# Kernel optimization log

Hardware: AMD Instinct MI355X
Metric: run time of the kernel (lower is better)

## Reference

```python
import jax, jax.numpy as jnp
import numpy as np

B, C, H, W = 4, 256, 64, 64
CR = max(C // 8, 1)  # reduced channels
EPS = 1e-12  # F.normalize eps


def setup_inputs() -> dict:
    key = jax.random.key(0)
    ks = jax.random.split(key, 8)
    s = 1.0 / np.sqrt(C)
    return {
        "x": jax.random.normal(ks[0], (B, C, H, W), dtype=jnp.float32),
        "Wq": jax.random.normal(ks[1], (CR, C), dtype=jnp.float32) * s,
        "bq": jax.random.normal(ks[2], (CR,), dtype=jnp.float32) * s,
        "Wk": jax.random.normal(ks[3], (CR, C), dtype=jnp.float32) * s,
        "bk": jax.random.normal(ks[4], (CR,), dtype=jnp.float32) * s,
        "Wv": jax.random.normal(ks[5], (C, C), dtype=jnp.float32) * s,
        "bv": jax.random.normal(ks[6], (C,), dtype=jnp.float32) * s,
        "gamma": jax.random.normal(ks[7], (1,), dtype=jnp.float32),
    }


def reference(x, Wq, bq, Wk, bk, Wv, bv, gamma):
    b, c, h, w = x.shape
    xf = x.reshape(b, c, h * w)  # [B, C, N]
    # 1x1 convs are per-pixel linear maps
    q = jnp.einsum("rc,bcn->brn", Wq, xf) + bq[None, :, None]  # [B, CR, N]
    k = jnp.einsum("rc,bcn->brn", Wk, xf) + bk[None, :, None]  # [B, CR, N]
    v = jnp.einsum("dc,bcn->bdn", Wv, xf) + bv[None, :, None]  # [B, C, N]
    # attention = bmm(key^T, query): [B, N, N]
    attn = jnp.einsum("brn,brm->bnm", k, q)
    attn = jax.nn.relu(attn)
    # L1 normalize along dim=1 (rows), matching F.normalize(p=1, dim=1)
    denom = jnp.maximum(jnp.sum(jnp.abs(attn), axis=1, keepdims=True), EPS)
    attn = attn / denom
    out = jnp.einsum("bcn,bnm->bcm", v, attn).reshape(b, c, h, w)
    return gamma[0] * out + x
```

## Files before the change

kernel.cpp:

```cpp
#include <hip/hip_runtime.h>
#include <hip/hip_bf16.h>

#define NB 4
#define NC 256
#define NN 4096
#define NCR 32

typedef __attribute__((ext_vector_type(8))) short short8_t;
typedef __attribute__((ext_vector_type(4))) float f32x4;
typedef __attribute__((ext_vector_type(2))) int int2_t;
typedef __attribute__((ext_vector_type(4))) int int4_t;
typedef __attribute__((ext_vector_type(4))) float float4_t;

static __device__ __forceinline__ unsigned short f2bf(float f) {
  unsigned u = __builtin_bit_cast(unsigned, f);
  u += 0x7FFFu + ((u >> 16) & 1u);
  return (unsigned short)(u >> 16);
}

static __device__ __forceinline__ unsigned cvt_pk(float lo, float hi) {
  unsigned r;
  asm("v_cvt_pk_bf16_f32 %0, %1, %2" : "=v"(r) : "v"(lo), "v"(hi));
  return r;
}

__global__ __launch_bounds__(64) void pack_w_kernel(
    const float* __restrict__ Wq, const float* __restrict__ Wk,
    const float* __restrict__ Wv, unsigned short* __restrict__ Wbf)
{
  const int row = blockIdx.x;
  const int t = threadIdx.x;
  const float* src = row < 32 ? Wq + (size_t)row * NC
                   : (row < 64 ? Wk + (size_t)(row - 32) * NC
                               : Wv + (size_t)(row - 64) * NC);
  float4_t v = *(const float4_t*)(src + t * 4);
  int2_t p;
  p[0] = cvt_pk(v[0], v[1]);
  p[1] = cvt_pk(v[2], v[3]);
  *(int2_t*)(Wbf + (size_t)row * NC + t * 4) = p;
}

__global__ __launch_bounds__(256) void qkv_kernel(
    const float* __restrict__ x, const unsigned short* __restrict__ Wbf,
    const float* __restrict__ bq, const float* __restrict__ bk,
    const float* __restrict__ bv,
    unsigned short* __restrict__ Qt, unsigned short* __restrict__ Kt,
    unsigned short* __restrict__ Vt)
{
  __shared__ unsigned short xT[2][64 * 32];

  const int bid = blockIdx.x;
  const int b   = bid >> 6;
  const int m0  = (bid & 63) * 64;
  const int tid = threadIdx.x;
  const int w    = tid >> 6;
  const int lane = tid & 63;
  const int lg   = lane >> 4;
  const int lm   = lane & 15;

  const float* xb = x + (size_t)b * NC * NN;
  const float* xld = xb + (size_t)(8 * w) * NN + m0 + lane;
  const int wofs = lane * 32 + ((w ^ (lane & 3)) << 3);
  const unsigned short* wrow = Wbf + (size_t)(w * 80 + lm) * NC;

  const f32x4 zero4 = {0.f, 0.f, 0.f, 0.f};
  f32x4 acc[5][4];
#pragma unroll
  for (int df = 0; df < 5; df++)
#pragma unroll
    for (int mf = 0; mf < 4; mf++) acc[df][mf] = zero4;

  float xg[8], xn[8];
#pragma unroll
  for (int j = 0; j < 8; j++) xg[j] = xld[j * NN];

#define QSTEP(KC, XC, XN, BUF) {                                              \
    if ((KC) < 7) {                                                           \
      _Pragma("unroll") for (int j = 0; j < 8; j++)                           \
        XN[j] = xld[(((KC) + 1) * 32 + j) * NN];                              \
    }                                                                         \
    short8_t wf[5];                                                           \
    _Pragma("unroll") for (int df = 0; df < 5; df++)                          \
      wf[df] = *(const short8_t*)(wrow + df * 16 * NC + (KC) * 32 + lg * 8);  \
    int4_t xw;                                                                \
    xw[0] = cvt_pk(XC[0], XC[1]); xw[1] = cvt_pk(XC[2], XC[3]);               \
    xw[2] = cvt_pk(XC[4], XC[5]); xw[3] = cvt_pk(XC[6], XC[7]);               \
    *(int4_t*)(&xT[BUF][wofs]) = xw;                                          \
    __syncthreads();                                                          \
    short8_t xf[4];                                                           \
    _Pragma("unroll") for (int mf = 0; mf < 4; mf++)                          \
      xf[mf] = *(const short8_t*)(&xT[BUF][(mf * 16 + lm) * 32 +              \
                                          ((lg ^ (lm & 3)) << 3)]);           \
    _Pragma("unroll") for (int df = 0; df < 5; df++)                          \
      _Pragma("unroll") for (int mf = 0; mf < 4; mf++)                        \
        acc[df][mf] = __builtin_amdgcn_mfma_f32_16x16x32_bf16(                \
            xf[mf], wf[df], acc[df][mf], 0, 0, 0);                            \
  }

#pragma unroll
  for (int kc = 0; kc < 8; kc += 2) {
    QSTEP(kc, xg, xn, 0)
    QSTEP(kc + 1, xn, xg, 1)
  }
#undef QSTEP

#pragma unroll
  for (int df = 0; df < 5; df++) {
    const int dbase = w * 80 + df * 16;
    if (dbase < 64) {
      const bool isq = dbase < 32;
      const float bia = isq ? bq[dbase + lm] : bk[dbase - 32 + lm];
      unsigned short* dst = isq ? Qt : Kt;
      const int dcol = (isq ? dbase : dbase - 32) + lm;
#pragma unroll
      for (int mf = 0; mf < 4; mf++)
#pragma unroll
        for (int i = 0; i < 4; i++) {
          const int m = m0 + mf * 16 + lg * 4 + i;
          dst[((size_t)b * NN + m) * NCR + dcol] = f2bf(acc[df][mf][i] + bia);
        }
    } else {
      const int c = dbase - 64 + lm;
      const float bia = bv[c];
#pragma unroll
      for (int mf = 0; mf < 4; mf++) {
        int2_t p;
        p[0] = cvt_pk(acc[df][mf][0] + bia, acc[df][mf][1] + bia);
        p[1] = cvt_pk(acc[df][mf][2] + bia, acc[df][mf][3] + bia);
        *(int2_t*)(Vt + ((size_t)b * NC + c) * NN + m0 + mf * 16 + lg * 4) = p;
      }
    }
  }
}

__global__ __launch_bounds__(256) void attn_kernel(
    const unsigned short* __restrict__ Qt, const unsigned short* __restrict__ Kt,
    const unsigned short* __restrict__ Vt, const float* __restrict__ x,
    const float* __restrict__ gamma, float* __restrict__ out)
{
  __shared__ unsigned short Slds[2][64 * 72];
  __shared__ float dlds[4][64];

  int bid = blockIdx.x;
  bid = (bid & 7) * 32 + (bid >> 3);
  const int b   = bid >> 6;
  const int m0  = (bid & 63) * 64;
  const int tid = threadIdx.x;
  const int w    = tid >> 6;
  const int lane = tid & 63;
  const int lg   = lane >> 4;
  const int lm   = lane & 15;

  const unsigned short* Qb = Qt + (size_t)b * NN * NCR;
  const unsigned short* Kb = Kt + (size_t)b * NN * NCR + (w * 16 + lm) * NCR + lg * 8;
  const unsigned short* Vb = Vt + (size_t)b * NC * NN;
  const unsigned short* pV[4];
#pragma unroll
  for (int cf = 0; cf < 4; cf++)
    pV[cf] = Vb + (size_t)(w * 64 + cf * 16 + lm) * NN + lg * 8;

  short8_t qf[4];
#pragma unroll
  for (int mf = 0; mf < 4; mf++)
    qf[mf] = *(const short8_t*)(Qb + (size_t)(m0 + mf * 16 + lm) * NCR + lg * 8);

  const f32x4 zero4 = {0.f, 0.f, 0.f, 0.f};
  f32x4 acc[4][4];
#pragma unroll
  for (int cf = 0; cf < 4; cf++)
#pragma unroll
    for (int mf = 0; mf < 4; mf++) acc[cf][mf] = zero4;
  float dsum[4] = {0.f, 0.f, 0.f, 0.f};

  short8_t kA, kB, vA[4][2], vB[4][2];
  kA = *(const short8_t*)(Kb);
#pragma unroll
  for (int cf = 0; cf < 4; cf++)
#pragma unroll
    for (int nch = 0; nch < 2; nch++)
      vA[cf][nch] = *(const short8_t*)(pV[cf] + nch * 32);

  const int swofs = w * 16 + lg * 4;

#define AITER(T, VC, VN, KC, KN, BUF) {                                       \
    const int n1 = (((T) + 1) & 63) * 64;                                     \
    KN = *(const short8_t*)(Kb + (size_t)n1 * NCR);                           \
    _Pragma("unroll") for (int cf = 0; cf < 4; cf++)                          \
      _Pragma("unroll") for (int nch = 0; nch < 2; nch++)                     \
        VN[cf][nch] = *(const short8_t*)(pV[cf] + n1 + nch * 32);             \
    _Pragma("unroll") for (int mf = 0; mf < 4; mf++) {                        \
      f32x4 s = __builtin_amdgcn_mfma_f32_16x16x32_bf16(KC, qf[mf], zero4, 0, 0, 0); \
      float s0 = fmaxf(s[0], 0.f), s1 = fmaxf(s[1], 0.f);                     \
      float s2 = fmaxf(s[2], 0.f), s3 = fmaxf(s[3], 0.f);                     \
      dsum[mf] += (s0 + s1) + (s2 + s3);                                      \
      int2_t p; p[0] = cvt_pk(s0, s1); p[1] = cvt_pk(s2, s3);                 \
      *(int2_t*)(&Slds[BUF][(mf * 16 + lm) * 72 + swofs]) = p;                \
    }                                                                         \
    __syncthreads();                                                          \
    _Pragma("unroll") for (int nch = 0; nch < 2; nch++) {                     \
      short8_t sf[4];                                                         \
      _Pragma("unroll") for (int mf = 0; mf < 4; mf++)                        \
        sf[mf] = *(const short8_t*)(&Slds[BUF][(mf * 16 + lm) * 72 + nch * 32 + lg * 8]); \
      _Pragma("unroll") for (int cf = 0; cf < 4; cf++)                        \
        _Pragma("unroll") for (int mf = 0; mf < 4; mf++)                      \
          acc[cf][mf] = __builtin_amdgcn_mfma_f32_16x16x32_bf16(              \
              VC[cf][nch], sf[mf], acc[cf][mf], 0, 0, 0);                     \
    }                                                                         \
  }

#pragma unroll 1
  for (int t = 0; t < 64; t += 2) {
    AITER(t, vA, vB, kA, kB, 0)
    AITER(t + 1, vB, vA, kB, kA, 1)
  }
#undef AITER

#pragma unroll
  for (int mf = 0; mf < 4; mf++) {
    float v = dsum[mf];
    v += __shfl_xor(v, 16);
    v += __shfl_xor(v, 32);
    dsum[mf] = v;
  }
  if (lane < 16) {
#pragma unroll
    for (int mf = 0; mf < 4; mf++) dlds[w][mf * 16 + lane] = dsum[mf];
  }
  __syncthreads();

  const float g0 = gamma[0];
  float rden[4];
#pragma unroll
  for (int mf = 0; mf < 4; mf++) {
    const int mloc = mf * 16 + lm;
    float den = dlds[0][mloc] + dlds[1][mloc] + dlds[2][mloc] + dlds[3][mloc];
    den = den > 1e-12f ? den : 1e-12f;
    rden[mf] = 1.0f / den;
  }

  const float* xb = x + (size_t)b * NC * NN;
  float* ob = out + (size_t)b * NC * NN;
#pragma unroll
  for (int cf = 0; cf < 4; cf++) {
#pragma unroll
    for (int i = 0; i < 4; i++) {
      const int c = w * 64 + cf * 16 + lg * 4 + i;
#pragma unroll
      for (int mf = 0; mf < 4; mf++) {
        const int m = m0 + mf * 16 + lm;
        ob[(size_t)c * NN + m] = g0 * acc[cf][mf][i] * rden[mf] + xb[(size_t)c * NN + m];
      }
    }
  }
}

extern "C" void kernel_launch(void* const* d_in, const int* in_sizes, int n_in,
                              void* d_out, int out_size, void* d_ws, size_t ws_size,
                              hipStream_t stream) {
  const float* x     = (const float*)d_in[0];
  const float* Wq    = (const float*)d_in[1];
  const float* bq    = (const float*)d_in[2];
  const float* Wk    = (const float*)d_in[3];
  const float* bk    = (const float*)d_in[4];
  const float* Wv    = (const float*)d_in[5];
  const float* bv    = (const float*)d_in[6];
  const float* gamma = (const float*)d_in[7];
  float* out = (float*)d_out;

  unsigned short* Wbf = (unsigned short*)d_ws;
  unsigned short* Qt  = Wbf + (size_t)320 * NC;
  unsigned short* Kt  = Qt + (size_t)NB * NN * NCR;
  unsigned short* Vt  = Kt + (size_t)NB * NN * NCR;

  hipLaunchKernelGGL(pack_w_kernel, dim3(320), dim3(64), 0, stream,
                     Wq, Wk, Wv, Wbf);
  hipLaunchKernelGGL(qkv_kernel, dim3(256), dim3(256), 0, stream,
                     x, Wbf, bq, bk, bv, Qt, Kt, Vt);
  hipLaunchKernelGGL(attn_kernel, dim3(256), dim3(256), 0, stream,
                     Qt, Kt, Vt, x, gamma, out);
}
```

Before: 88.24 us.

## Split attention key range across 8 waves and halve QKV tile per block

The attention kernel now runs 512 threads per block. Waves 4-7 process the second half of each 128-key tile, and the two halves' accumulators are reduced through LDS at the end, with s_setprio raised around the MFMA phase. The QKV projection kernel uses 32-pixel tiles over 512 blocks with a wider K chunk and a new swizzle. The aim is more waves in flight to hide the latency of V/K loads on a 256-block grid, at the cost of extra LDS traffic and synchronisation for the cross-wave reduction.

After: 211.7 us. 2.4x slower.

```diff
diff --git a/kernel.cpp b/kernel.cpp
--- a/kernel.cpp
+++ b/kernel.cpp
@@ -5,6 +5,7 @@
 #define NC 256
 #define NN 4096
 #define NCR 32
+#define PITCH 136
 
 typedef __attribute__((ext_vector_type(8))) short short8_t;
 typedef __attribute__((ext_vector_type(4))) float f32x4;
@@ -40,69 +41,72 @@
   *(int2_t*)(Wbf + (size_t)row * NC + t * 4) = p;
 }
 
-__global__ __launch_bounds__(256) void qkv_kernel(
+__global__ __launch_bounds__(256, 2) void qkv_kernel(
     const float* __restrict__ x, const unsigned short* __restrict__ Wbf,
     const float* __restrict__ bq, const float* __restrict__ bk,
     const float* __restrict__ bv,
     unsigned short* __restrict__ Qt, unsigned short* __restrict__ Kt,
     unsigned short* __restrict__ Vt)
 {
-  __shared__ unsigned short xT[2][64 * 32];
+  __shared__ unsigned short xT[2][32 * 64];
 
   const int bid = blockIdx.x;
-  const int b   = bid >> 6;
-  const int m0  = (bid & 63) * 64;
+  const int b   = bid >> 7;
+  const int m0  = (bid & 127) * 32;
   const int tid = threadIdx.x;
   const int w    = tid >> 6;
   const int lane = tid & 63;
   const int lg   = lane >> 4;
   const int lm   = lane & 15;
 
-  const float* xb = x + (size_t)b * NC * NN;
-  const float* xld = xb + (size_t)(8 * w) * NN + m0 + lane;
-  const int wofs = lane * 32 + ((w ^ (lane & 3)) << 3);
+  const int mcol = tid & 31, kg = tid >> 5;
+  const float* xld = x + (size_t)b * NC * NN + (size_t)(kg * 8) * NN + m0 + mcol;
+  const int wofs = mcol * 64 + ((kg ^ (mcol & 7)) << 3);
   const unsigned short* wrow = Wbf + (size_t)(w * 80 + lm) * NC;
 
   const f32x4 zero4 = {0.f, 0.f, 0.f, 0.f};
-  f32x4 acc[5][4];
+  f32x4 acc[5][2];
 #pragma unroll
   for (int df = 0; df < 5; df++)
 #pragma unroll
-    for (int mf = 0; mf < 4; mf++) acc[df][mf] = zero4;
+    for (int mf = 0; mf < 2; mf++) acc[df][mf] = zero4;
 
   float xg[8], xn[8];
 #pragma unroll
-  for (int j = 0; j < 8; j++) xg[j] = xld[j * NN];
-
-#define QSTEP(KC, XC, XN, BUF) {                                              \
-    if ((KC) < 7) {                                                           \
+  for (int j = 0; j < 8; j++) xg[j] = xld[(size_t)j * NN];
+
+#define QCHUNK(C, XC, XN, BUF) {                                              \
+    if ((C) < 3) {                                                            \
       _Pragma("unroll") for (int j = 0; j < 8; j++)                           \
-        XN[j] = xld[(((KC) + 1) * 32 + j) * NN];                              \
+        XN[j] = xld[(size_t)(((C) + 1) * 64 + j) * NN];                       \
     }                                                                         \
-    short8_t wf[5];                                                           \
-    _Pragma("unroll") for (int df = 0; df < 5; df++)                          \
-      wf[df] = *(const short8_t*)(wrow + df * 16 * NC + (KC) * 32 + lg * 8);  \
-    int4_t xw;                                                                \
-    xw[0] = cvt_pk(XC[0], XC[1]); xw[1] = cvt_pk(XC[2], XC[3]);               \
-    xw[2] = cvt_pk(XC[4], XC[5]); xw[3] = cvt_pk(XC[6], XC[7]);               \
-    *(int4_t*)(&xT[BUF][wofs]) = xw;                                          \
+    int4_t xwv;                                                               \
+    xwv[0] = cvt_pk(XC[0], XC[1]); xwv[1] = cvt_pk(XC[2], XC[3]);             \
+    xwv[2] = cvt_pk(XC[4], XC[5]); xwv[3] = cvt_pk(XC[6], XC[7]);             \
+    *(int4_t*)(&xT[BUF][wofs]) = xwv;                                         \
     __syncthreads();                                                          \
-    short8_t xf[4];                                                           \
-    _Pragma("unroll") for (int mf = 0; mf < 4; mf++)                          \
-      xf[mf] = *(const short8_t*)(&xT[BUF][(mf * 16 + lm) * 32 +              \
-                                          ((lg ^ (lm & 3)) << 3)]);           \
-    _Pragma("unroll") for (int df = 0; df < 5; df++)                          \
-      _Pragma("unroll") for (int mf = 0; mf < 4; mf++)                        \
-        acc[df][mf] = __builtin_amdgcn_mfma_f32_16x16x32_bf16(                \
-            xf[mf], wf[df], acc[df][mf], 0, 0, 0);                            \
-  }
-
-#pragma unroll
-  for (int kc = 0; kc < 8; kc += 2) {
-    QSTEP(kc, xg, xn, 0)
-    QSTEP(kc + 1, xn, xg, 1)
-  }
-#undef QSTEP
+    _Pragma("unroll") for (int ks = 0; ks < 2; ks++) {                        \
+      short8_t xf[2];                                                         \
+      _Pragma("unroll") for (int mf = 0; mf < 2; mf++) {                      \
+        const int row = mf * 16 + lm;                                         \
+        const int unit = (ks * 4 + lg) ^ (lm & 7);                            \
+        xf[mf] = *(const short8_t*)(&xT[BUF][row * 64 + unit * 8]);           \
+      }                                                                       \
+      _Pragma("unroll") for (int df = 0; df < 5; df++) {                      \
+        const short8_t wf = *(const short8_t*)(wrow + (size_t)df * 16 * NC +  \
+                                               (C) * 64 + ks * 32 + lg * 8);  \
+        _Pragma("unroll") for (int mf = 0; mf < 2; mf++)                      \
+          acc[df][mf] = __builtin_amdgcn_mfma_f32_16x16x32_bf16(              \
+              xf[mf], wf, acc[df][mf], 0, 0, 0);                              \
+      }                                                                       \
+    }                                                                         \
+  }
+
+  QCHUNK(0, xg, xn, 0)
+  QCHUNK(1, xn, xg, 1)
+  QCHUNK(2, xg, xn, 0)
+  QCHUNK(3, xn, xg, 1)
+#undef QCHUNK
 
 #pragma unroll
   for (int df = 0; df < 5; df++) {
@@ -113,7 +117,7 @@
       unsigned short* dst = isq ? Qt : Kt;
       const int dcol = (isq ? dbase : dbase - 32) + lm;
 #pragma unroll
-      for (int mf = 0; mf < 4; mf++)
+      for (int mf = 0; mf < 2; mf++)
 #pragma unroll
         for (int i = 0; i < 4; i++) {
           const int m = m0 + mf * 16 + lg * 4 + i;
@@ -123,7 +127,7 @@
       const int c = dbase - 64 + lm;
       const float bia = bv[c];
 #pragma unroll
-      for (int mf = 0; mf < 4; mf++) {
+      for (int mf = 0; mf < 2; mf++) {
         int2_t p;
         p[0] = cvt_pk(acc[df][mf][0] + bia, acc[df][mf][1] + bia);
         p[1] = cvt_pk(acc[df][mf][2] + bia, acc[df][mf][3] + bia);
@@ -133,13 +137,14 @@
   }
 }
 
-__global__ __launch_bounds__(256) void attn_kernel(
+__global__ __launch_bounds__(512, 2) void attn_kernel(
     const unsigned short* __restrict__ Qt, const unsigned short* __restrict__ Kt,
     const unsigned short* __restrict__ Vt, const float* __restrict__ x,
     const float* __restrict__ gamma, float* __restrict__ out)
 {
-  __shared__ unsigned short Slds[2][64 * 72];
-  __shared__ float dlds[4][64];
+  __shared__ unsigned short Slds[2][64 * PITCH];
+  __shared__ float mbuf[4][64][17];
+  __shared__ float dlds[8][64];
 
   int bid = blockIdx.x;
   bid = (bid & 7) * 32 + (bid >> 3);
@@ -150,14 +155,17 @@
   const int lane = tid & 63;
   const int lg   = lane >> 4;
   const int lm   = lane & 15;
+  const int cg   = w & 3;
+  const int nh   = w >> 2;
 
   const unsigned short* Qb = Qt + (size_t)b * NN * NCR;
-  const unsigned short* Kb = Kt + (size_t)b * NN * NCR + (w * 16 + lm) * NCR + lg * 8;
+  const unsigned short* Kp = Kt + (size_t)b * NN * NCR +
+                             (size_t)(w * 16 + lm) * NCR + lg * 8;
   const unsigned short* Vb = Vt + (size_t)b * NC * NN;
   const unsigned short* pV[4];
 #pragma unroll
   for (int cf = 0; cf < 4; cf++)
-    pV[cf] = Vb + (size_t)(w * 64 + cf * 16 + lm) * NN + lg * 8;
+    pV[cf] = Vb + (size_t)(cg * 64 + cf * 16 + lm) * NN + nh * 64 + lg * 8;
 
   short8_t qf[4];
 #pragma unroll
@@ -173,7 +181,7 @@
   float dsum[4] = {0.f, 0.f, 0.f, 0.f};
 
   short8_t kA, kB, vA[4][2], vB[4][2];
-  kA = *(const short8_t*)(Kb);
+  kA = *(const short8_t*)(Kp);
 #pragma unroll
   for (int cf = 0; cf < 4; cf++)
 #pragma unroll
@@ -182,9 +190,9 @@
 
   const int swofs = w * 16 + lg * 4;
 
-#define AITER(T, VC, VN, KC, KN, BUF) {                                       \
-    const int n1 = (((T) + 1) & 63) * 64;                                     \
-    KN = *(const short8_t*)(Kb + (size_t)n1 * NCR);                           \
+#define AITER(T, KC, KN, VC, VN, BUF) {                                       \
+    const int n1 = (((T) + 1) & 31) * 128;                                    \
+    KN = *(const short8_t*)(Kp + (size_t)n1 * NCR);                           \
     _Pragma("unroll") for (int cf = 0; cf < 4; cf++)                          \
       _Pragma("unroll") for (int nch = 0; nch < 2; nch++)                     \
         VN[cf][nch] = *(const short8_t*)(pV[cf] + n1 + nch * 32);             \
@@ -194,24 +202,27 @@
       float s2 = fmaxf(s[2], 0.f), s3 = fmaxf(s[3], 0.f);                     \
       dsum[mf] += (s0 + s1) + (s2 + s3);                                      \
       int2_t p; p[0] = cvt_pk(s0, s1); p[1] = cvt_pk(s2, s3);                 \
-      *(int2_t*)(&Slds[BUF][(mf * 16 + lm) * 72 + swofs]) = p;                \
+      *(int2_t*)(&Slds[BUF][(mf * 16 + lm) * PITCH + swofs]) = p;             \
     }                                                                         \
     __syncthreads();                                                          \
+    __builtin_amdgcn_s_setprio(1);                                            \
     _Pragma("unroll") for (int nch = 0; nch < 2; nch++) {                     \
       short8_t sf[4];                                                         \
       _Pragma("unroll") for (int mf = 0; mf < 4; mf++)                        \
-        sf[mf] = *(const short8_t*)(&Slds[BUF][(mf * 16 + lm) * 72 + nch * 32 + lg * 8]); \
+        sf[mf] = *(const short8_t*)(&Slds[BUF][(mf * 16 + lm) * PITCH +       \
+                                              nh * 64 + nch * 32 + lg * 8]);  \
       _Pragma("unroll") for (int cf = 0; cf < 4; cf++)                        \
         _Pragma("unroll") for (int mf = 0; mf < 4; mf++)                      \
           acc[cf][mf] = __builtin_amdgcn_mfma_f32_16x16x32_bf16(              \
               VC[cf][nch], sf[mf], acc[cf][mf], 0, 0, 0);                     \
     }                                                                         \
+    __builtin_amdgcn_s_setprio(0);                                            \
   }
 
 #pragma unroll 1
-  for (int t = 0; t < 64; t += 2) {
-    AITER(t, vA, vB, kA, kB, 0)
-    AITER(t + 1, vB, vA, kB, kA, 1)
+  for (int t = 0; t < 32; t += 2) {
+    AITER(t, kA, kB, vA, vB, 0)
+    AITER(t + 1, kB, kA, vB, vA, 1)
   }
 #undef AITER
 
@@ -220,31 +231,65 @@
     float v = dsum[mf];
     v += __shfl_xor(v, 16);
     v += __shfl_xor(v, 32);
-    dsum[mf] = v;
-  }
-  if (lane < 16) {
-#pragma unroll
-    for (int mf = 0; mf < 4; mf++) dlds[w][mf * 16 + lane] = dsum[mf];
-  }
-  __syncthreads();
+    if (lane < 16) dlds[w][mf * 16 + lane] = v;
+  }
+
+#pragma unroll
+  for (int cf = 0; cf < 2; cf++) {
+    if (w >= 4) {
+#pragma unroll
+      for (int mf = 0; mf < 4; mf++)
+#pragma unroll
+        for (int i = 0; i < 4; i++) mbuf[w - 4][lane][mf * 4 + i] = acc[cf][mf][i];
+    }
+    __syncthreads();
+    if (w < 4) {
+#pragma unroll
+      for (int mf = 0; mf < 4; mf++)
+#pragma unroll
+        for (int i = 0; i < 4; i++) acc[cf][mf][i] += mbuf[w][lane][mf * 4 + i];
+    }
+    __syncthreads();
+  }
+#pragma unroll
+  for (int cf = 2; cf < 4; cf++) {
+    if (w < 4) {
+#pragma unroll
+      for (int mf = 0; mf < 4; mf++)
+#pragma unroll
+        for (int i = 0; i < 4; i++) mbuf[w][lane][mf * 4 + i] = acc[cf][mf][i];
+    }
+    __syncthreads();
+    if (w >= 4) {
+#pragma unroll
+      for (int mf = 0; mf < 4; mf++)
+#pragma unroll
+        for (int i = 0; i < 4; i++) acc[cf][mf][i] += mbuf[w - 4][lane][mf * 4 + i];
+    }
+    __syncthreads();
+  }
 
   const float g0 = gamma[0];
   float rden[4];
 #pragma unroll
   for (int mf = 0; mf < 4; mf++) {
     const int mloc = mf * 16 + lm;
-    float den = dlds[0][mloc] + dlds[1][mloc] + dlds[2][mloc] + dlds[3][mloc];
+    float den = 0.f;
+#pragma unroll
+    for (int ww = 0; ww < 8; ww++) den += dlds[ww][mloc];
     den = den > 1e-12f ? den : 1e-12f;
     rden[mf] = 1.0f / den;
   }
 
+  const int cf0 = (w >> 2) * 2;
   const float* xb = x + (size_t)b * NC * NN;
   float* ob = out + (size_t)b * NC * NN;
 #pragma unroll
-  for (int cf = 0; cf < 4; cf++) {
+  for (int cfo = 0; cfo < 2; cfo++) {
+    const int cf = cf0 + cfo;
 #pragma unroll
     for (int i = 0; i < 4; i++) {
-      const int c = w * 64 + cf * 16 + lg * 4 + i;
+      const int c = cg * 64 + cf * 16 + lg * 4 + i;
 #pragma unroll
       for (int mf = 0; mf < 4; mf++) {
         const int m = m0 + mf * 16 + lm;
@@ -274,8 +319,8 @@
 
   hipLaunchKernelGGL(pack_w_kernel, dim3(320), dim3(64), 0, stream,
                      Wq, Wk, Wv, Wbf);
-  hipLaunchKernelGGL(qkv_kernel, dim3(256), dim3(256), 0, stream,
+  hipLaunchKernelGGL(qkv_kernel, dim3(512), dim3(256), 0, stream,
                      x, Wbf, bq, bk, bv, Qt, Kt, Vt);
-  hipLaunchKernelGGL(attn_kernel, dim3(256), dim3(256), 0, stream,
+  hipLaunchKernelGGL(attn_kernel, dim3(256), dim3(512), 0, stream,
                      Qt, Kt, Vt, x, gamma, out);
 }
```
